# Optimization experiments

Measured on AMD Instinct MI355X. Metric: run time of the kernel, lower is better.

## Reference

```python
import jax, jax.numpy as jnp
import numpy as np

N = 10000       # n_nodes
E = 640000      # n_edges (avg degree 64)
D_IN = 128      # in_feats
D_H = 128       # n_hidden
N_CLS = 64      # n_classes


def setup_inputs() -> dict:
    key = jax.random.key(0)
    k1, k2, k3, k4, k5, k6 = jax.random.split(key, 6)
    features = jax.random.normal(k1, (N, D_IN), dtype=jnp.float32)
    src = jax.random.randint(k2, (E,), 0, N, dtype=jnp.int32)
    dst = jax.random.randint(k3, (E,), 0, N, dtype=jnp.int32)
    s = 0.05  # small init scale to keep activations bounded across 3 layers
    # Stored as [in, out]; equivalent to torch Linear weight [out, in] transposed.
    W0 = jax.random.normal(k4, (D_IN, D_H), dtype=jnp.float32) * s
    W1 = jax.random.normal(k5, (D_H, D_H), dtype=jnp.float32) * s
    W2 = jax.random.normal(k6, (D_H, N_CLS), dtype=jnp.float32) * s
    return {"features": features, "W0": W0, "W1": W1, "W2": W2,
            "src": src, "dst": dst}


def reference(features, W0, W1, W2, src, dst):
    # GINConv with aggregator 'sum', eps=0 (learn_eps=False):
    #   h' = Linear(h + sum_{(u->v) in E} h[u] scattered to v)
    # Dropout is identity at inference; 'activation' is unused in the module.
    def gin_layer(h, W):
        agg = jax.ops.segment_sum(h[src], dst, num_segments=N)  # [N, d]
        return (h + agg) @ W

    h = gin_layer(features, W0)
    h = gin_layer(h, W1)
    h = gin_layer(h, W2)
    return h
```

## Files before the change

### kernel.cpp

```cpp
#include <hip/hip_runtime.h>
#include <hip/hip_bf16.h>

#define NN 10000
#define NE 640000
#define D_IN 128
#define D_H 128
#define N_CLS 64
#define CAP 160
#define GRP 157
#define CAPC 4800
#define CCS 16
#define SENT 10000
#define EPB 1024
#define AB 625
#define CB 1251
#define W01B 16
#define WPB 4

__device__ __forceinline__ float blo(unsigned u) { return __uint_as_float(u << 16); }
__device__ __forceinline__ float bhi(unsigned u) { return __uint_as_float(u & 0xffff0000u); }
__device__ __forceinline__ unsigned short f2bf(float f) {
    unsigned u = __float_as_uint(f);
    return (unsigned short)((u + 0x7fffu + ((u >> 16) & 1u)) >> 16);
}
__device__ __forceinline__ unsigned packbf(float a, float b) {
    return (unsigned)f2bf(a) | ((unsigned)f2bf(b) << 16);
}

__global__ __launch_bounds__(256) void prep_a(const int* __restrict__ src,
                                              const int* __restrict__ dst,
                                              int* __restrict__ coarse_cnt,
                                              unsigned* __restrict__ coarse,
                                              const float* __restrict__ feat,
                                              unsigned* __restrict__ hb0,
                                              const float* __restrict__ W0,
                                              const float* __restrict__ W1,
                                              float* __restrict__ W01) {
    int bid = blockIdx.x;
    if (bid >= AB + CB) {
        int t = (bid - AB - CB) * 256 + threadIdx.x;
        int i = t >> 5;
        int jb = (t & 31) << 2;
        float c0 = 0.f, c1 = 0.f, c2 = 0.f, c3 = 0.f;
        for (int k = 0; k < 128; ++k) {
            float a = W0[i * 128 + k];
            float4 b = *(const float4*)&W1[k * 128 + jb];
            c0 += a * b.x; c1 += a * b.y; c2 += a * b.z; c3 += a * b.w;
        }
        *(float4*)&W01[i * 128 + jb] = make_float4(c0, c1, c2, c3);
        return;
    }
    if (bid >= AB) {
        int t = (bid - AB) * 256 + threadIdx.x;
        if (t < NN * 32) {
            float4 f = ((const float4*)feat)[t];
            ((uint2*)hb0)[t] = make_uint2(packbf(f.x, f.y), packbf(f.z, f.w));
        } else if (t < (NN + 1) * 32) {
            ((uint2*)hb0)[t] = make_uint2(0u, 0u);
        }
        return;
    }
    __shared__ unsigned stage[EPB];
    __shared__ int hist[GRP], gbase[GRP], cur[GRP];
    const int t = threadIdx.x;
    for (int i = t; i < GRP; i += 256) hist[i] = 0;
    __syncthreads();
    const int e0 = bid * EPB;
    for (int i = t; i < EPB; i += 256) {
        int s = src[e0 + i];
        int d = dst[e0 + i];
        stage[i] = (unsigned)s | ((unsigned)d << 16);
        atomicAdd(&hist[d >> 6], 1);
    }
    __syncthreads();
    for (int i = t; i < GRP; i += 256) {
        gbase[i] = atomicAdd(&coarse_cnt[i * CCS], hist[i]);
        cur[i] = 0;
    }
    __syncthreads();
    for (int i = t; i < EPB; i += 256) {
        unsigned u = stage[i];
        int g = u >> 22;
        int r = atomicAdd(&cur[g], 1);
        coarse[g * CAPC + gbase[g] + r] = u;
    }
}

__global__ __launch_bounds__(1024) void prep_b(const int* __restrict__ coarse_cnt,
                                               const unsigned* __restrict__ coarse,
                                               int* __restrict__ cnt,
                                               unsigned short* __restrict__ colbuf,
                                               const float* __restrict__ W01,
                                               const float* __restrict__ W2,
                                               unsigned* __restrict__ wbp) {
    const int g = blockIdx.x;
    const int t = threadIdx.x;
    if (g >= GRP) {
        int s = (g - GRP) * 1024 + t;
        int kp = s >> 6, j = s & 63;
        float c0 = 0.f, c1 = 0.f;
        const float* r0 = W01 + (2 * kp) * 128;
        const float* r1 = r0 + 128;
        for (int k = 0; k < 128; ++k) {
            float w2 = W2[k * 64 + j];
            c0 += r0[k] * w2;
            c1 += r1[k] * w2;
        }
        wbp[kp * 64 + j] = packbf(c0, c1);
        return;
    }
    __shared__ int cur[64];
    __shared__ unsigned short sbuf[64][CAP];
    if (t < 64) cur[t] = 0;
    __syncthreads();
    const int m = coarse_cnt[g * CCS];
    const unsigned* cb = coarse + g * CAPC;
    for (int i = t; i < m; i += 1024) {
        unsigned u = cb[i];
        int s = (int)(u & 0xFFFFu);
        int dl = (int)(u >> 16) - (g << 6);
        int r = atomicAdd(&cur[dl], 1);
        sbuf[dl][r] = (unsigned short)s;
    }
    __syncthreads();
    if (t < 64) {
        int n = (g << 6) + t;
        if (n < NN) {
            int c = cur[t];
            int pad = (32 - (c & 31)) & 31;
            for (int k = 0; k < pad; ++k) sbuf[t][c + k] = (unsigned short)SENT;
            cnt[n] = c + pad;
        }
    }
    __syncthreads();
    const uint4* s4 = (const uint4*)sbuf;
    for (int idx = t; idx < 64 * (CAP / 8); idx += 1024) {
        int node = (g << 6) + (idx / (CAP / 8));
        if (node < NN)
            ((uint4*)colbuf)[(size_t)node * (CAP / 8) + (idx % (CAP / 8))] = s4[idx];
    }
}

__global__ __launch_bounds__(256, 4) void proj1(const uint4* __restrict__ hb4,
                                                const int* __restrict__ cnt,
                                                const unsigned short* __restrict__ colbuf,
                                                const unsigned* __restrict__ Wbp,
                                                unsigned short* __restrict__ tb) {
    constexpr int M = 4;
    __shared__ float xs[M][D_H];
    const int base = blockIdx.x * M;
    const int tid = threadIdx.x;
    const int wave = tid >> 6;
    const int lane = tid & 63;
    const int sub = lane >> 4;
    const int off = lane & 15;

    const int n = __builtin_amdgcn_readfirstlane(base + wave);
    float a0, a1, a2, a3, a4, a5, a6, a7;
    if (sub == 0) {
        uint4 u = hb4[n * 16 + off];
        a0 = blo(u.x); a1 = bhi(u.x); a2 = blo(u.y); a3 = bhi(u.y);
        a4 = blo(u.z); a5 = bhi(u.z); a6 = blo(u.w); a7 = bhi(u.w);
    } else {
        a0 = a1 = a2 = a3 = a4 = a5 = a6 = a7 = 0.f;
    }
    const int NCH = __builtin_amdgcn_readfirstlane(cnt[n]) >> 5;
    const uint2* cl = (const uint2*)(colbuf + n * CAP);
    const int sh = (sub & 1) << 4;
    uint2 p0 = cl[0], p1 = cl[1], p2 = cl[2], p3 = cl[3];
    uint2 p4 = cl[4], p5 = cl[5], p6 = cl[6], p7 = cl[7];
    for (int c = 0; c < NCH; ++c) {
        unsigned w0 = (sub & 2) ? p0.y : p0.x;
        unsigned w1 = (sub & 2) ? p1.y : p1.x;
        unsigned w2 = (sub & 2) ? p2.y : p2.x;
        unsigned w3 = (sub & 2) ? p3.y : p3.x;
        unsigned w4 = (sub & 2) ? p4.y : p4.x;
        unsigned w5 = (sub & 2) ? p5.y : p5.x;
        unsigned w6 = (sub & 2) ? p6.y : p6.x;
        unsigned w7 = (sub & 2) ? p7.y : p7.x;
        int s0 = (int)((w0 >> sh) & 0xffffu);
        int s1 = (int)((w1 >> sh) & 0xffffu);
        int s2 = (int)((w2 >> sh) & 0xffffu);
        int s3 = (int)((w3 >> sh) & 0xffffu);
        int s4 = (int)((w4 >> sh) & 0xffffu);
        int s5 = (int)((w5 >> sh) & 0xffffu);
        int s6 = (int)((w6 >> sh) & 0xffffu);
        int s7 = (int)((w7 >> sh) & 0xffffu);
        uint4 u0 = hb4[s0 * 16 + off];
        uint4 u1 = hb4[s1 * 16 + off];
        uint4 u2 = hb4[s2 * 16 + off];
        uint4 u3 = hb4[s3 * 16 + off];
        uint4 u4 = hb4[s4 * 16 + off];
        uint4 u5 = hb4[s5 * 16 + off];
        uint4 u6 = hb4[s6 * 16 + off];
        uint4 u7 = hb4[s7 * 16 + off];
        {
            const uint2* nx = cl + 8 * (c + 1);
            p0 = nx[0]; p1 = nx[1]; p2 = nx[2]; p3 = nx[3];
            p4 = nx[4]; p5 = nx[5]; p6 = nx[6]; p7 = nx[7];
        }
        a0 += ((blo(u0.x) + blo(u1.x)) + (blo(u2.x) + blo(u3.x)))
            + ((blo(u4.x) + blo(u5.x)) + (blo(u6.x) + blo(u7.x)));
        a1 += ((bhi(u0.x) + bhi(u1.x)) + (bhi(u2.x) + bhi(u3.x)))
            + ((bhi(u4.x) + bhi(u5.x)) + (bhi(u6.x) + bhi(u7.x)));
        a2 += ((blo(u0.y) + blo(u1.y)) + (blo(u2.y) + blo(u3.y)))
            + ((blo(u4.y) + blo(u5.y)) + (blo(u6.y) + blo(u7.y)));
        a3 += ((bhi(u0.y) + bhi(u1.y)) + (bhi(u2.y) + bhi(u3.y)))
            + ((bhi(u4.y) + bhi(u5.y)) + (bhi(u6.y) + bhi(u7.y)));
        a4 += ((blo(u0.z) + blo(u1.z)) + (blo(u2.z) + blo(u3.z)))
            + ((blo(u4.z) + blo(u5.z)) + (blo(u6.z) + blo(u7.z)));
        a5 += ((bhi(u0.z) + bhi(u1.z)) + (bhi(u2.z) + bhi(u3.z)))
            + ((bhi(u4.z) + bhi(u5.z)) + (bhi(u6.z) + bhi(u7.z)));
        a6 += ((blo(u0.w) + blo(u1.w)) + (blo(u2.w) + blo(u3.w)))
            + ((blo(u4.w) + blo(u5.w)) + (blo(u6.w) + blo(u7.w)));
        a7 += ((bhi(u0.w) + bhi(u1.w)) + (bhi(u2.w) + bhi(u3.w)))
            + ((bhi(u4.w) + bhi(u5.w)) + (bhi(u6.w) + bhi(u7.w)));
    }
    a0 += __shfl_xor(a0, 16); a0 += __shfl_xor(a0, 32);
    a1 += __shfl_xor(a1, 16); a1 += __shfl_xor(a1, 32);
    a2 += __shfl_xor(a2, 16); a2 += __shfl_xor(a2, 32);
    a3 += __shfl_xor(a3, 16); a3 += __shfl_xor(a3, 32);
    a4 += __shfl_xor(a4, 16); a4 += __shfl_xor(a4, 32);
    a5 += __shfl_xor(a5, 16); a5 += __shfl_xor(a5, 32);
    a6 += __shfl_xor(a6, 16); a6 += __shfl_xor(a6, 32);
    a7 += __shfl_xor(a7, 16); a7 += __shfl_xor(a7, 32);
    if (sub == 0) {
        *(float4*)&xs[wave][8 * off]     = make_float4(a0, a1, a2, a3);
        *(float4*)&xs[wave][8 * off + 4] = make_float4(a4, a5, a6, a7);
    }
    __syncthreads();

    const int j = tid & 63;
    float acc = 0.f;
    for (int k = 0; k < D_H; k += 4) {
        unsigned wp0 = Wbp[(k >> 1) * 64 + j];
        unsigned wp1 = Wbp[((k >> 1) + 1) * 64 + j];
        float w0 = blo(wp0), w1 = bhi(wp0), w2 = blo(wp1), w3 = bhi(wp1);
        float4 xv = *(const float4*)&xs[wave][k];
        acc += xv.x * w0 + xv.y * w1 + xv.z * w2 + xv.w * w3;
    }
    tb[(size_t)(base + wave) * 64 + j] = f2bf(acc);
    if (blockIdx.x == 0 && tid < 16) {
        ((uint2*)(tb + (size_t)SENT * 64))[tid] = make_uint2(0u, 0u);
    }
}

__global__ __launch_bounds__(256, 4) void agg64b(const uint4* __restrict__ tb4,
                                                 const int* __restrict__ cnt,
                                                 const unsigned short* __restrict__ colbuf,
                                                 unsigned short* __restrict__ tb2) {
    constexpr int M = 4;
    const int base = blockIdx.x * M;
    const int tid = threadIdx.x;
    const int wave = tid >> 6;
    const int lane = tid & 63;
    const int sub = lane >> 3;
    const int off = lane & 7;

    const int n = __builtin_amdgcn_readfirstlane(base + wave);
    float a0, a1, a2, a3, a4, a5, a6, a7;
    if (sub == 0) {
        uint4 u = tb4[n * 8 + off];
        a0 = blo(u.x); a1 = bhi(u.x); a2 = blo(u.y); a3 = bhi(u.y);
        a4 = blo(u.z); a5 = bhi(u.z); a6 = blo(u.w); a7 = bhi(u.w);
    } else {
        a0 = a1 = a2 = a3 = a4 = a5 = a6 = a7 = 0.f;
    }
    const int NCH = __builtin_amdgcn_readfirstlane(cnt[n]) >> 5;
    const uint2* cl = (const uint2*)(colbuf + n * CAP);
    const int hi4 = sub >> 2;
    const int wsel = (sub >> 1) & 1;
    const int sh = (sub & 1) << 4;
    uint2 p0 = cl[0], p1 = cl[1], p2 = cl[2], p3 = cl[3];
    uint2 p4 = cl[4], p5 = cl[5], p6 = cl[6], p7 = cl[7];
    for (int c = 0; c < NCH; ++c) {
        unsigned q0 = hi4 ? (wsel ? p1.y : p1.x) : (wsel ? p0.y : p0.x);
        unsigned q1 = hi4 ? (wsel ? p3.y : p3.x) : (wsel ? p2.y : p2.x);
        unsigned q2 = hi4 ? (wsel ? p5.y : p5.x) : (wsel ? p4.y : p4.x);
        unsigned q3 = hi4 ? (wsel ? p7.y : p7.x) : (wsel ? p6.y : p6.x);
        int s0 = (int)((q0 >> sh) & 0xffffu);
        int s1 = (int)((q1 >> sh) & 0xffffu);
        int s2 = (int)((q2 >> sh) & 0xffffu);
        int s3 = (int)((q3 >> sh) & 0xffffu);
        uint4 u0 = tb4[s0 * 8 + off];
        uint4 u1 = tb4[s1 * 8 + off];
        uint4 u2 = tb4[s2 * 8 + off];
        uint4 u3 = tb4[s3 * 8 + off];
        {
            const uint2* nx = cl + 8 * (c + 1);
            p0 = nx[0]; p1 = nx[1]; p2 = nx[2]; p3 = nx[3];
            p4 = nx[4]; p5 = nx[5]; p6 = nx[6]; p7 = nx[7];
        }
        a0 += (blo(u0.x) + blo(u1.x)) + (blo(u2.x) + blo(u3.x));
        a1 += (bhi(u0.x) + bhi(u1.x)) + (bhi(u2.x) + bhi(u3.x));
        a2 += (blo(u0.y) + blo(u1.y)) + (blo(u2.y) + blo(u3.y));
        a3 += (bhi(u0.y) + bhi(u1.y)) + (bhi(u2.y) + bhi(u3.y));
        a4 += (blo(u0.z) + blo(u1.z)) + (blo(u2.z) + blo(u3.z));
        a5 += (bhi(u0.z) + bhi(u1.z)) + (bhi(u2.z) + bhi(u3.z));
        a6 += (blo(u0.w) + blo(u1.w)) + (blo(u2.w) + blo(u3.w));
        a7 += (bhi(u0.w) + bhi(u1.w)) + (bhi(u2.w) + bhi(u3.w));
    }
    a0 += __shfl_xor(a0, 8); a0 += __shfl_xor(a0, 16); a0 += __shfl_xor(a0, 32);
    a1 += __shfl_xor(a1, 8); a1 += __shfl_xor(a1, 16); a1 += __shfl_xor(a1, 32);
    a2 += __shfl_xor(a2, 8); a2 += __shfl_xor(a2, 16); a2 += __shfl_xor(a2, 32);
    a3 += __shfl_xor(a3, 8); a3 += __shfl_xor(a3, 16); a3 += __shfl_xor(a3, 32);
    a4 += __shfl_xor(a4, 8); a4 += __shfl_xor(a4, 16); a4 += __shfl_xor(a4, 32);
    a5 += __shfl_xor(a5, 8); a5 += __shfl_xor(a5, 16); a5 += __shfl_xor(a5, 32);
    a6 += __shfl_xor(a6, 8); a6 += __shfl_xor(a6, 16); a6 += __shfl_xor(a6, 32);
    a7 += __shfl_xor(a7, 8); a7 += __shfl_xor(a7, 16); a7 += __shfl_xor(a7, 32);
    if (sub == 0) {
        unsigned short* o = tb2 + (size_t)n * 64 + 8 * off;
        *(uint4*)o = make_uint4(packbf(a0, a1), packbf(a2, a3),
                                packbf(a4, a5), packbf(a6, a7));
    }
    if (blockIdx.x == 0 && tid < 16) {
        ((uint2*)(tb2 + (size_t)SENT * 64))[tid] = make_uint2(0u, 0u);
    }
}

__global__ __launch_bounds__(256, 4) void agg64f(const uint4* __restrict__ tb4,
                                                 const int* __restrict__ cnt,
                                                 const unsigned short* __restrict__ colbuf,
                                                 float* __restrict__ outf) {
    constexpr int M = 4;
    const int base = blockIdx.x * M;
    const int tid = threadIdx.x;
    const int wave = tid >> 6;
    const int lane = tid & 63;
    const int sub = lane >> 3;
    const int off = lane & 7;

    const int n = __builtin_amdgcn_readfirstlane(base + wave);
    float a0, a1, a2, a3, a4, a5, a6, a7;
    if (sub == 0) {
        uint4 u = tb4[n * 8 + off];
        a0 = blo(u.x); a1 = bhi(u.x); a2 = blo(u.y); a3 = bhi(u.y);
        a4 = blo(u.z); a5 = bhi(u.z); a6 = blo(u.w); a7 = bhi(u.w);
    } else {
        a0 = a1 = a2 = a3 = a4 = a5 = a6 = a7 = 0.f;
    }
    const int NCH = __builtin_amdgcn_readfirstlane(cnt[n]) >> 5;
    const uint2* cl = (const uint2*)(colbuf + n * CAP);
    const int hi4 = sub >> 2;
    const int wsel = (sub >> 1) & 1;
    const int sh = (sub & 1) << 4;
    uint2 p0 = cl[0], p1 = cl[1], p2 = cl[2], p3 = cl[3];
    uint2 p4 = cl[4], p5 = cl[5], p6 = cl[6], p7 = cl[7];
    for (int c = 0; c < NCH; ++c) {
        unsigned q0 = hi4 ? (wsel ? p1.y : p1.x) : (wsel ? p0.y : p0.x);
        unsigned q1 = hi4 ? (wsel ? p3.y : p3.x) : (wsel ? p2.y : p2.x);
        unsigned q2 = hi4 ? (wsel ? p5.y : p5.x) : (wsel ? p4.y : p4.x);
        unsigned q3 = hi4 ? (wsel ? p7.y : p7.x) : (wsel ? p6.y : p6.x);
        int s0 = (int)((q0 >> sh) & 0xffffu);
        int s1 = (int)((q1 >> sh) & 0xffffu);
        int s2 = (int)((q2 >> sh) & 0xffffu);
        int s3 = (int)((q3 >> sh) & 0xffffu);
        uint4 u0 = tb4[s0 * 8 + off];
        uint4 u1 = tb4[s1 * 8 + off];
        uint4 u2 = tb4[s2 * 8 + off];
        uint4 u3 = tb4[s3 * 8 + off];
        {
            const uint2* nx = cl + 8 * (c + 1);
            p0 = nx[0]; p1 = nx[1]; p2 = nx[2]; p3 = nx[3];
            p4 = nx[4]; p5 = nx[5]; p6 = nx[6]; p7 = nx[7];
        }
        a0 += (blo(u0.x) + blo(u1.x)) + (blo(u2.x) + blo(u3.x));
        a1 += (bhi(u0.x) + bhi(u1.x)) + (bhi(u2.x) + bhi(u3.x));
        a2 += (blo(u0.y) + blo(u1.y)) + (blo(u2.y) + blo(u3.y));
        a3 += (bhi(u0.y) + bhi(u1.y)) + (bhi(u2.y) + bhi(u3.y));
        a4 += (blo(u0.z) + blo(u1.z)) + (blo(u2.z) + blo(u3.z));
        a5 += (bhi(u0.z) + bhi(u1.z)) + (bhi(u2.z) + bhi(u3.z));
        a6 += (blo(u0.w) + blo(u1.w)) + (blo(u2.w) + blo(u3.w));
        a7 += (bhi(u0.w) + bhi(u1.w)) + (bhi(u2.w) + bhi(u3.w));
    }
    a0 += __shfl_xor(a0, 8); a0 += __shfl_xor(a0, 16); a0 += __shfl_xor(a0, 32);
    a1 += __shfl_xor(a1, 8); a1 += __shfl_xor(a1, 16); a1 += __shfl_xor(a1, 32);
    a2 += __shfl_xor(a2, 8); a2 += __shfl_xor(a2, 16); a2 += __shfl_xor(a2, 32);
    a3 += __shfl_xor(a3, 8); a3 += __shfl_xor(a3, 16); a3 += __shfl_xor(a3, 32);
    a4 += __shfl_xor(a4, 8); a4 += __shfl_xor(a4, 16); a4 += __shfl_xor(a4, 32);
    a5 += __shfl_xor(a5, 8); a5 += __shfl_xor(a5, 16); a5 += __shfl_xor(a5, 32);
    a6 += __shfl_xor(a6, 8); a6 += __shfl_xor(a6, 16); a6 += __shfl_xor(a6, 32);
    a7 += __shfl_xor(a7, 8); a7 += __shfl_xor(a7, 16); a7 += __shfl_xor(a7, 32);
    if (sub == 0) {
        float* o = outf + (size_t)n * N_CLS + 8 * off;
        *(float4*)o       = make_float4(a0, a1, a2, a3);
        *(float4*)(o + 4) = make_float4(a4, a5, a6, a7);
    }
}

extern "C" void kernel_launch(void* const* d_in, const int* in_sizes, int n_in,
                              void* d_out, int out_size, void* d_ws, size_t ws_size,
                              hipStream_t stream) {
    const float* feat = (const float*)d_in[0];
    const float* W0   = (const float*)d_in[1];
    const float* W1   = (const float*)d_in[2];
    const float* W2   = (const float*)d_in[3];
    const int*   src  = (const int*)d_in[4];
    const int*   dst  = (const int*)d_in[5];
    float* out = (float*)d_out;

    int* coarse_cnt        = (int*)d_ws;
    int* cnt               = coarse_cnt + GRP * CCS;
    unsigned short* colbuf = (unsigned short*)(cnt + NN + 8);
    unsigned* coarse       = (unsigned*)(colbuf + (size_t)NN * CAP);
    unsigned* hb0          = coarse + (size_t)GRP * CAPC;
    unsigned* tbu          = hb0 + (size_t)(NN + 1) * 64;
    unsigned* tb2u         = tbu + (size_t)(NN + 1) * 32;
    float* W01             = (float*)(tb2u + (size_t)(NN + 1) * 32);
    unsigned* wbp          = (unsigned*)(W01 + 16384);
    unsigned short* tb     = (unsigned short*)tbu;
    unsigned short* tb2    = (unsigned short*)tb2u;

    hipMemsetAsync(coarse_cnt, 0, GRP * CCS * sizeof(int), stream);
    prep_a<<<AB + CB + W01B, 256, 0, stream>>>(src, dst, coarse_cnt, coarse, feat, hb0,
                                               W0, W1, W01);
    prep_b<<<GRP + WPB, 1024, 0, stream>>>(coarse_cnt, coarse, cnt, colbuf,
                                           W01, W2, wbp);

    proj1<<<NN / 4, 256, 0, stream>>>((const uint4*)hb0, cnt, colbuf, wbp, tb);
    agg64b<<<NN / 4, 256, 0, stream>>>((const uint4*)tb, cnt, colbuf, tb2);
    agg64f<<<NN / 4, 256, 0, stream>>>((const uint4*)tb2, cnt, colbuf, out);
}
```

Before: 139.8 us.

## Project features to 64 dims before first aggregation, reuse 64-wide agg kernel

Because the whole network is linear, the first layer now multiplies the raw features by the combined weight before aggregating, instead of aggregating 128-wide bf16 rows and then projecting. That halves the bytes gathered per edge in the first aggregation, which now reuses the existing 64-wide agg64b kernel. It also drops the bf16 conversion pass over the features from prep_a. In exchange there is one extra kernel launch (a small dense GEMM), and the rounding order changes slightly because the projection now happens before the sum.

```diff
diff --git a/kernel.cpp b/kernel.cpp
--- a/kernel.cpp
+++ b/kernel.cpp
@@ -13,7 +13,6 @@
 #define SENT 10000
 #define EPB 1024
 #define AB 625
-#define CB 1251
 #define W01B 16
 #define WPB 4
 
@@ -31,14 +30,12 @@
                                               const int* __restrict__ dst,
                                               int* __restrict__ coarse_cnt,
                                               unsigned* __restrict__ coarse,
-                                              const float* __restrict__ feat,
-                                              unsigned* __restrict__ hb0,
                                               const float* __restrict__ W0,
                                               const float* __restrict__ W1,
                                               float* __restrict__ W01) {
     int bid = blockIdx.x;
-    if (bid >= AB + CB) {
-        int t = (bid - AB - CB) * 256 + threadIdx.x;
+    if (bid >= AB) {
+        int t = (bid - AB) * 256 + threadIdx.x;
         int i = t >> 5;
         int jb = (t & 31) << 2;
         float c0 = 0.f, c1 = 0.f, c2 = 0.f, c3 = 0.f;
@@ -48,16 +45,6 @@
             c0 += a * b.x; c1 += a * b.y; c2 += a * b.z; c3 += a * b.w;
         }
         *(float4*)&W01[i * 128 + jb] = make_float4(c0, c1, c2, c3);
-        return;
-    }
-    if (bid >= AB) {
-        int t = (bid - AB) * 256 + threadIdx.x;
-        if (t < NN * 32) {
-            float4 f = ((const float4*)feat)[t];
-            ((uint2*)hb0)[t] = make_uint2(packbf(f.x, f.y), packbf(f.z, f.w));
-        } else if (t < (NN + 1) * 32) {
-            ((uint2*)hb0)[t] = make_uint2(0u, 0u);
-        }
         return;
     }
     __shared__ unsigned stage[EPB];
@@ -141,107 +128,29 @@
     }
 }
 
-__global__ __launch_bounds__(256, 4) void proj1(const uint4* __restrict__ hb4,
-                                                const int* __restrict__ cnt,
-                                                const unsigned short* __restrict__ colbuf,
+__global__ __launch_bounds__(256, 4) void gemm0(const float* __restrict__ feat,
                                                 const unsigned* __restrict__ Wbp,
-                                                unsigned short* __restrict__ tb) {
-    constexpr int M = 4;
-    __shared__ float xs[M][D_H];
-    const int base = blockIdx.x * M;
+                                                unsigned short* __restrict__ g0) {
+    __shared__ float xs[4][128];
     const int tid = threadIdx.x;
     const int wave = tid >> 6;
     const int lane = tid & 63;
-    const int sub = lane >> 4;
-    const int off = lane & 15;
-
-    const int n = __builtin_amdgcn_readfirstlane(base + wave);
-    float a0, a1, a2, a3, a4, a5, a6, a7;
-    if (sub == 0) {
-        uint4 u = hb4[n * 16 + off];
-        a0 = blo(u.x); a1 = bhi(u.x); a2 = blo(u.y); a3 = bhi(u.y);
-        a4 = blo(u.z); a5 = bhi(u.z); a6 = blo(u.w); a7 = bhi(u.w);
-    } else {
-        a0 = a1 = a2 = a3 = a4 = a5 = a6 = a7 = 0.f;
-    }
-    const int NCH = __builtin_amdgcn_readfirstlane(cnt[n]) >> 5;
-    const uint2* cl = (const uint2*)(colbuf + n * CAP);
-    const int sh = (sub & 1) << 4;
-    uint2 p0 = cl[0], p1 = cl[1], p2 = cl[2], p3 = cl[3];
-    uint2 p4 = cl[4], p5 = cl[5], p6 = cl[6], p7 = cl[7];
-    for (int c = 0; c < NCH; ++c) {
-        unsigned w0 = (sub & 2) ? p0.y : p0.x;
-        unsigned w1 = (sub & 2) ? p1.y : p1.x;
-        unsigned w2 = (sub & 2) ? p2.y : p2.x;
-        unsigned w3 = (sub & 2) ? p3.y : p3.x;
-        unsigned w4 = (sub & 2) ? p4.y : p4.x;
-        unsigned w5 = (sub & 2) ? p5.y : p5.x;
-        unsigned w6 = (sub & 2) ? p6.y : p6.x;
-        unsigned w7 = (sub & 2) ? p7.y : p7.x;
-        int s0 = (int)((w0 >> sh) & 0xffffu);
-        int s1 = (int)((w1 >> sh) & 0xffffu);
-        int s2 = (int)((w2 >> sh) & 0xffffu);
-        int s3 = (int)((w3 >> sh) & 0xffffu);
-        int s4 = (int)((w4 >> sh) & 0xffffu);
-        int s5 = (int)((w5 >> sh) & 0xffffu);
-        int s6 = (int)((w6 >> sh) & 0xffffu);
-        int s7 = (int)((w7 >> sh) & 0xffffu);
-        uint4 u0 = hb4[s0 * 16 + off];
-        uint4 u1 = hb4[s1 * 16 + off];
-        uint4 u2 = hb4[s2 * 16 + off];
-        uint4 u3 = hb4[s3 * 16 + off];
-        uint4 u4 = hb4[s4 * 16 + off];
-        uint4 u5 = hb4[s5 * 16 + off];
-        uint4 u6 = hb4[s6 * 16 + off];
-        uint4 u7 = hb4[s7 * 16 + off];
-        {
-            const uint2* nx = cl + 8 * (c + 1);
-            p0 = nx[0]; p1 = nx[1]; p2 = nx[2]; p3 = nx[3];
-            p4 = nx[4]; p5 = nx[5]; p6 = nx[6]; p7 = nx[7];
-        }
-        a0 += ((blo(u0.x) + blo(u1.x)) + (blo(u2.x) + blo(u3.x)))
-            + ((blo(u4.x) + blo(u5.x)) + (blo(u6.x) + blo(u7.x)));
-        a1 += ((bhi(u0.x) + bhi(u1.x)) + (bhi(u2.x) + bhi(u3.x)))
-            + ((bhi(u4.x) + bhi(u5.x)) + (bhi(u6.x) + bhi(u7.x)));
-        a2 += ((blo(u0.y) + blo(u1.y)) + (blo(u2.y) + blo(u3.y)))
-            + ((blo(u4.y) + blo(u5.y)) + (blo(u6.y) + blo(u7.y)));
-        a3 += ((bhi(u0.y) + bhi(u1.y)) + (bhi(u2.y) + bhi(u3.y)))
-            + ((bhi(u4.y) + bhi(u5.y)) + (bhi(u6.y) + bhi(u7.y)));
-        a4 += ((blo(u0.z) + blo(u1.z)) + (blo(u2.z) + blo(u3.z)))
-            + ((blo(u4.z) + blo(u5.z)) + (blo(u6.z) + blo(u7.z)));
-        a5 += ((bhi(u0.z) + bhi(u1.z)) + (bhi(u2.z) + bhi(u3.z)))
-            + ((bhi(u4.z) + bhi(u5.z)) + (bhi(u6.z) + bhi(u7.z)));
-        a6 += ((blo(u0.w) + blo(u1.w)) + (blo(u2.w) + blo(u3.w)))
-            + ((blo(u4.w) + blo(u5.w)) + (blo(u6.w) + blo(u7.w)));
-        a7 += ((bhi(u0.w) + bhi(u1.w)) + (bhi(u2.w) + bhi(u3.w)))
-            + ((bhi(u4.w) + bhi(u5.w)) + (bhi(u6.w) + bhi(u7.w)));
-    }
-    a0 += __shfl_xor(a0, 16); a0 += __shfl_xor(a0, 32);
-    a1 += __shfl_xor(a1, 16); a1 += __shfl_xor(a1, 32);
-    a2 += __shfl_xor(a2, 16); a2 += __shfl_xor(a2, 32);
-    a3 += __shfl_xor(a3, 16); a3 += __shfl_xor(a3, 32);
-    a4 += __shfl_xor(a4, 16); a4 += __shfl_xor(a4, 32);
-    a5 += __shfl_xor(a5, 16); a5 += __shfl_xor(a5, 32);
-    a6 += __shfl_xor(a6, 16); a6 += __shfl_xor(a6, 32);
-    a7 += __shfl_xor(a7, 16); a7 += __shfl_xor(a7, 32);
-    if (sub == 0) {
-        *(float4*)&xs[wave][8 * off]     = make_float4(a0, a1, a2, a3);
-        *(float4*)&xs[wave][8 * off + 4] = make_float4(a4, a5, a6, a7);
-    }
-    __syncthreads();
-
-    const int j = tid & 63;
+    const int n = blockIdx.x * 4 + wave;
+    float2 f = *(const float2*)&feat[(size_t)n * 128 + lane * 2];
+    xs[wave][lane * 2]     = f.x;
+    xs[wave][lane * 2 + 1] = f.y;
+    __syncthreads();
+    const int j = lane;
     float acc = 0.f;
-    for (int k = 0; k < D_H; k += 4) {
+    for (int k = 0; k < 128; k += 4) {
         unsigned wp0 = Wbp[(k >> 1) * 64 + j];
         unsigned wp1 = Wbp[((k >> 1) + 1) * 64 + j];
-        float w0 = blo(wp0), w1 = bhi(wp0), w2 = blo(wp1), w3 = bhi(wp1);
         float4 xv = *(const float4*)&xs[wave][k];
-        acc += xv.x * w0 + xv.y * w1 + xv.z * w2 + xv.w * w3;
-    }
-    tb[(size_t)(base + wave) * 64 + j] = f2bf(acc);
+        acc += xv.x * blo(wp0) + xv.y * bhi(wp0) + xv.z * blo(wp1) + xv.w * bhi(wp1);
+    }
+    g0[(size_t)n * 64 + j] = f2bf(acc);
     if (blockIdx.x == 0 && tid < 16) {
-        ((uint2*)(tb + (size_t)SENT * 64))[tid] = make_uint2(0u, 0u);
+        ((uint2*)(g0 + (size_t)SENT * 64))[tid] = make_uint2(0u, 0u);
     }
 }
 
@@ -403,21 +312,22 @@
     int* cnt               = coarse_cnt + GRP * CCS;
     unsigned short* colbuf = (unsigned short*)(cnt + NN + 8);
     unsigned* coarse       = (unsigned*)(colbuf + (size_t)NN * CAP);
-    unsigned* hb0          = coarse + (size_t)GRP * CAPC;
-    unsigned* tbu          = hb0 + (size_t)(NN + 1) * 64;
+    unsigned* g0u          = coarse + (size_t)GRP * CAPC;
+    unsigned* tbu          = g0u + (size_t)(NN + 1) * 32;
     unsigned* tb2u         = tbu + (size_t)(NN + 1) * 32;
     float* W01             = (float*)(tb2u + (size_t)(NN + 1) * 32);
     unsigned* wbp          = (unsigned*)(W01 + 16384);
+    unsigned short* g0     = (unsigned short*)g0u;
     unsigned short* tb     = (unsigned short*)tbu;
     unsigned short* tb2    = (unsigned short*)tb2u;
 
     hipMemsetAsync(coarse_cnt, 0, GRP * CCS * sizeof(int), stream);
-    prep_a<<<AB + CB + W01B, 256, 0, stream>>>(src, dst, coarse_cnt, coarse, feat, hb0,
-                                               W0, W1, W01);
+    prep_a<<<AB + W01B, 256, 0, stream>>>(src, dst, coarse_cnt, coarse, W0, W1, W01);
     prep_b<<<GRP + WPB, 1024, 0, stream>>>(coarse_cnt, coarse, cnt, colbuf,
                                            W01, W2, wbp);
 
-    proj1<<<NN / 4, 256, 0, stream>>>((const uint4*)hb0, cnt, colbuf, wbp, tb);
+    gemm0<<<NN / 4, 256, 0, stream>>>(feat, wbp, g0);
+    agg64b<<<NN / 4, 256, 0, stream>>>((const uint4*)g0, cnt, colbuf, tb);
     agg64b<<<NN / 4, 256, 0, stream>>>((const uint4*)tb, cnt, colbuf, tb2);
     agg64f<<<NN / 4, 256, 0, stream>>>((const uint4*)tb2, cnt, colbuf, out);
 }
```

New measurement: 137.2 us. Within noise of the previous version (-1.9%).
